# Kernel optimization log

Measured on AMD Instinct MI355X. Metric: run time of the kernel, lower is better.

## Reference

```python
import jax, jax.numpy as jnp
import numpy as np
import math

E = 1024      # embed_dim
H = 16        # num_heads
D = 32        # head_dim = E // H // 2
DEPTH = 12
LAMBDA_INIT = 0.8 - 0.6 * math.exp(-0.3 * DEPTH)
B, T = 4, 1024
EPS = 1e-5


def setup_inputs() -> dict:
    key = jax.random.key(0)
    ks = jax.random.split(key, 10)
    s = 0.02  # realistic init scale for weight matrices
    return {
        "x": jax.random.normal(ks[0], (B, T, E), jnp.float32),
        "Wq": jax.random.normal(ks[1], (E, E), jnp.float32) * s,
        "Wk": jax.random.normal(ks[2], (E, E), jnp.float32) * s,
        "Wv": jax.random.normal(ks[3], (E, E), jnp.float32) * s,
        "Wo": jax.random.normal(ks[4], (E, E), jnp.float32) * s,
        "lambda_q1": jax.random.normal(ks[5], (D,), jnp.float32) * 0.1,
        "lambda_k1": jax.random.normal(ks[6], (D,), jnp.float32) * 0.1,
        "lambda_q2": jax.random.normal(ks[7], (D,), jnp.float32) * 0.1,
        "lambda_k2": jax.random.normal(ks[8], (D,), jnp.float32) * 0.1,
        "g": jnp.ones((2 * D,), jnp.float32),  # subln affine weight
    }


def reference(x, Wq, Wk, Wv, Wo, lambda_q1, lambda_k1, lambda_q2, lambda_k2, g):
    b, t, _ = x.shape
    scaling = D ** -0.5
    # projections (torch Linear: x @ W.T), split into 2H half-width q/k heads
    q = (x @ Wq.T).reshape(b, t, 2 * H, D).transpose(0, 2, 1, 3) * scaling  # [b,2H,t,D]
    k = (x @ Wk.T).reshape(b, t, 2 * H, D).transpose(0, 2, 1, 3)            # [b,2H,t,D]
    v = (x @ Wv.T).reshape(b, t, H, 2 * D).transpose(0, 2, 1, 3)            # [b,H,t,2D]
    # dual score maps, fp32 softmax
    aw = jnp.einsum('bhqd,bhkd->bhqk', q, k)               # [b,2H,t,t]
    aw = jnp.nan_to_num(aw)
    aw = jax.nn.softmax(aw.astype(jnp.float32), axis=-1).astype(q.dtype)
    # scalar lambda
    lam1 = jnp.exp(jnp.sum(lambda_q1 * lambda_k1))
    lam2 = jnp.exp(jnp.sum(lambda_q2 * lambda_k2))
    lam = lam1 - lam2 + LAMBDA_INIT
    # differential subtract of the paired softmax maps
    aw = aw.reshape(b, H, 2, t, t)
    aw = aw[:, :, 0] - lam * aw[:, :, 1]                   # [b,H,t,t]
    attn = jnp.einsum('bhqk,bhkd->bhqd', aw, v)            # [b,H,t,2D]
    # per-head RMSNorm over 2D channel dim (affine)
    attn = attn * jax.lax.rsqrt(jnp.mean(attn * attn, axis=-1, keepdims=True) + EPS) * g
    attn = attn * (1.0 - LAMBDA_INIT)
    attn = attn.transpose(0, 2, 1, 3).reshape(b, t, H * 2 * D)  # [b,t,E]
    return attn @ Wo.T
```

## Files before the change

kernel.cpp:

```cpp
#include <hip/hip_runtime.h>
#include <math.h>

#define E_   1024
#define H_   16
#define B_   4
#define T_   1024
#define LAMBDA_INIT 0.783605766532f
#define SCALE_Q 0.17677669529663687f

typedef short s16x8 __attribute__((ext_vector_type(8)));
typedef float f32x4 __attribute__((ext_vector_type(4)));

__device__ inline ushort f2bf(float x) {
    unsigned u = __builtin_bit_cast(unsigned, x);
    u += 0x7fffu + ((u >> 16) & 1u);
    return (ushort)(u >> 16);
}

__device__ inline void gl_lds16(const ushort* g, ushort* l) {
    __builtin_amdgcn_global_load_lds((const __attribute__((address_space(1))) void*)g,
                                     (__attribute__((address_space(3))) void*)l,
                                     16, 0, 0);
}

__global__ __launch_bounds__(256) void cast_x(const float* __restrict__ in,
                                              ushort* __restrict__ out)
{
    int i = (blockIdx.x * 256 + threadIdx.x) * 8;
    float4 a = *(const float4*)&in[i];
    float4 b = *(const float4*)&in[i + 4];
    union { ushort u[8]; uint4 v; } o;
    o.u[0] = f2bf(a.x); o.u[1] = f2bf(a.y); o.u[2] = f2bf(a.z); o.u[3] = f2bf(a.w);
    o.u[4] = f2bf(b.x); o.u[5] = f2bf(b.y); o.u[6] = f2bf(b.z); o.u[7] = f2bf(b.w);
    *(uint4*)&out[i] = o.v;
}

__global__ __launch_bounds__(256) void cast_w4(
    const float* __restrict__ w0, const float* __restrict__ w1,
    const float* __restrict__ w2, const float* __restrict__ w3,
    ushort* __restrict__ o0, ushort* __restrict__ o1,
    ushort* __restrict__ o2, ushort* __restrict__ o3)
{
    const float* in = blockIdx.y == 0 ? w0 : (blockIdx.y == 1 ? w1 : (blockIdx.y == 2 ? w2 : w3));
    ushort* out = blockIdx.y == 0 ? o0 : (blockIdx.y == 1 ? o1 : (blockIdx.y == 2 ? o2 : o3));
    int i = (blockIdx.x * 256 + threadIdx.x) * 8;
    float4 a = *(const float4*)&in[i];
    float4 b = *(const float4*)&in[i + 4];
    union { ushort u[8]; uint4 v; } o;
    o.u[0] = f2bf(a.x); o.u[1] = f2bf(a.y); o.u[2] = f2bf(a.z); o.u[3] = f2bf(a.w);
    o.u[4] = f2bf(b.x); o.u[5] = f2bf(b.y); o.u[6] = f2bf(b.z); o.u[7] = f2bf(b.w);
    *(uint4*)&out[i] = o.v;
}

__global__ void lam_kernel(const float* __restrict__ lq1, const float* __restrict__ lk1,
                           const float* __restrict__ lq2, const float* __restrict__ lk2,
                           float* __restrict__ lamp)
{
    int l = threadIdx.x;
    float p1 = 0.f, p2 = 0.f;
    if (l < 32) { p1 = lq1[l] * lk1[l]; p2 = lq2[l] * lk2[l]; }
    #pragma unroll
    for (int off = 32; off; off >>= 1) {
        p1 += __shfl_xor(p1, off);
        p2 += __shfl_xor(p2, off);
    }
    if (l == 0) lamp[0] = expf(p1) - expf(p2) + LAMBDA_INIT;
}

__global__ __launch_bounds__(256) void gemm_qkv(
    const ushort* __restrict__ Xb, const ushort* __restrict__ Wqb,
    const ushort* __restrict__ Wkb, const ushort* __restrict__ Wvb,
    ushort* __restrict__ QKV)
{
    __shared__ ushort As[128 * 32];
    __shared__ ushort Ws[128 * 32];
    const int tid = threadIdx.x;
    const int wave = tid >> 6, lane = tid & 63;
    const int l15 = lane & 15, quad = lane >> 4;
    const int bm = blockIdx.y * 128;
    const int bng = blockIdx.x * 128;
    const int region = bng >> 10;
    const ushort* W = region == 0 ? Wqb : (region == 1 ? Wkb : Wvb);
    const float scale = region == 0 ? SCALE_Q : 1.0f;
    const int wn = bng & 1023;
    const int lrow = lane >> 2;
    const int lcol = (lane & 3) * 8;

    f32x4 acc[4][4] = {};
    const int wr = wave >> 1, wc = wave & 1;

    for (int k0 = 0; k0 < 1024; k0 += 32) {
        #pragma unroll
        for (int p = 0; p < 2; ++p) {
            int i = wave + 4 * p;
            gl_lds16(&Xb[(size_t)(bm + i * 16 + lrow) * 1024 + k0 + lcol], &As[i * 512]);
            gl_lds16(&W [(size_t)(wn + i * 16 + lrow) * 1024 + k0 + lcol], &Ws[i * 512]);
        }
        __syncthreads();
        s16x8 a[4], b[4];
        #pragma unroll
        for (int i = 0; i < 4; ++i)
            a[i] = *(const s16x8*)&As[(wr * 64 + i * 16 + l15) * 32 + quad * 8];
        #pragma unroll
        for (int j = 0; j < 4; ++j)
            b[j] = *(const s16x8*)&Ws[(wc * 64 + j * 16 + l15) * 32 + quad * 8];
        #pragma unroll
        for (int i = 0; i < 4; ++i)
            #pragma unroll
            for (int j = 0; j < 4; ++j)
                acc[i][j] = __builtin_amdgcn_mfma_f32_16x16x32_bf16(a[i], b[j], acc[i][j], 0, 0, 0);
        __syncthreads();
    }

    #pragma unroll
    for (int i = 0; i < 4; ++i)
        #pragma unroll
        for (int j = 0; j < 4; ++j)
            #pragma unroll
            for (int r = 0; r < 4; ++r) {
                int row = bm + wr * 64 + i * 16 + quad * 4 + r;
                int col = bng + wc * 64 + j * 16 + l15;
                QKV[(size_t)row * 3072 + col] = f2bf(acc[i][j][r] * scale);
            }
}

__global__ __launch_bounds__(256) void gemm_out(
    const ushort* __restrict__ Ab, const ushort* __restrict__ Wob,
    float* __restrict__ C)
{
    __shared__ ushort As[64 * 32];
    __shared__ ushort Ws[128 * 32];
    const int tid = threadIdx.x;
    const int wave = tid >> 6, lane = tid & 63;
    const int l15 = lane & 15, quad = lane >> 4;
    const int bm = blockIdx.y * 64;
    const int bn = blockIdx.x * 128;
    const int lrow = lane >> 2;
    const int lcol = (lane & 3) * 8;

    f32x4 acc[2][4] = {};
    const int wr = wave >> 1, wc = wave & 1;

    for (int k0 = 0; k0 < 1024; k0 += 32) {
        gl_lds16(&Ab[(size_t)(bm + wave * 16 + lrow) * 1024 + k0 + lcol], &As[wave * 512]);
        #pragma unroll
        for (int p = 0; p < 2; ++p) {
            int i = wave + 4 * p;
            gl_lds16(&Wob[(size_t)(bn + i * 16 + lrow) * 1024 + k0 + lcol], &Ws[i * 512]);
        }
        __syncthreads();
        s16x8 a[2], b[4];
        #pragma unroll
        for (int i = 0; i < 2; ++i)
            a[i] = *(const s16x8*)&As[(wr * 32 + i * 16 + l15) * 32 + quad * 8];
        #pragma unroll
        for (int j = 0; j < 4; ++j)
            b[j] = *(const s16x8*)&Ws[(wc * 64 + j * 16 + l15) * 32 + quad * 8];
        #pragma unroll
        for (int i = 0; i < 2; ++i)
            #pragma unroll
            for (int j = 0; j < 4; ++j)
                acc[i][j] = __builtin_amdgcn_mfma_f32_16x16x32_bf16(a[i], b[j], acc[i][j], 0, 0, 0);
        __syncthreads();
    }

    #pragma unroll
    for (int i = 0; i < 2; ++i)
        #pragma unroll
        for (int j = 0; j < 4; ++j)
            #pragma unroll
            for (int r = 0; r < 4; ++r) {
                int row = bm + wr * 32 + i * 16 + quad * 4 + r;
                int col = bn + wc * 64 + j * 16 + l15;
                C[(size_t)row * 1024 + col] = acc[i][j][r];
            }
}

__global__ __launch_bounds__(256) void diff_attn(
    const ushort* __restrict__ QKV, const float* __restrict__ g,
    const float* __restrict__ lamp, ushort* __restrict__ O)
{
    __shared__ __align__(16) ushort QsVt[64][72];
    __shared__ __align__(16) ushort Ks[64][72];
    __shared__ __align__(16) ushort Vs[64][72];
    __shared__ __align__(16) ushort Ps[4][16][72];

    const int tid  = threadIdx.x;
    const int lane = tid & 63;
    const int wave = tid >> 6;
    const int l15  = lane & 15;
    const int quad = lane >> 4;

    const int blk = blockIdx.x;
    const int qt = blk & 15;
    const int h  = (blk >> 4) & 15;
    const int b  = blk >> 8;
    const int q0 = qt * 64;
    const int hoff = h * 64;
    const size_t rowbase = (size_t)b * T_;

    const ushort* Qg = QKV;
    const ushort* Kg = QKV + 1024;
    const ushort* Vg = QKV + 2048;

    #pragma unroll
    for (int p = 0; p < 2; ++p) {
        int idx = tid + 256 * p;
        int r = idx >> 3, seg = idx & 7;
        *(uint4*)&QsVt[r][seg * 8] =
            *(const uint4*)&Qg[(rowbase + q0 + r) * 3072 + hoff + seg * 8];
    }
    const float lam = lamp[0];
    float gv[4];
    #pragma unroll
    for (int j = 0; j < 4; ++j) gv[j] = g[j * 16 + l15];
    __syncthreads();

    s16x8 aq[2];
    #pragma unroll
    for (int c = 0; c < 2; ++c)
        aq[c] = *(const s16x8*)&QsVt[wave * 16 + l15][c * 32 + quad * 8];

    const f32x4 zf = {0.f, 0.f, 0.f, 0.f};
    f32x4 o0[4] = {zf, zf, zf, zf};
    f32x4 o1[4] = {zf, zf, zf, zf};
    float lsum[2][4] = {};

    for (int kt = 0; kt < T_ / 64; ++kt) {
        __syncthreads();
        #pragma unroll
        for (int p = 0; p < 2; ++p) {
            int idx = tid + 256 * p;
            int r = idx >> 3, seg = idx & 7;
            size_t gro = (rowbase + kt * 64 + r) * 3072 + hoff + seg * 8;
            *(uint4*)&Ks[r][seg * 8] = *(const uint4*)&Kg[gro];
            *(uint4*)&Vs[r][seg * 8] = *(const uint4*)&Vg[gro];
        }
        __syncthreads();

        f32x4 S[2][4];
        #pragma unroll
        for (int c = 0; c < 2; ++c)
            #pragma unroll
            for (int j = 0; j < 4; ++j) {
                s16x8 bk = *(const s16x8*)&Ks[j * 16 + l15][c * 32 + quad * 8];
                S[c][j] = __builtin_amdgcn_mfma_f32_16x16x32_bf16(aq[c], bk, zf, 0, 0, 0);
            }

        #pragma unroll
        for (int p = 0; p < 2; ++p) {
            int idx = tid + 256 * p;
            int vc = idx & 63, n8 = (idx >> 6) * 8;
            union { ushort u[8]; uint4 v4; } tmp;
            #pragma unroll
            for (int i = 0; i < 8; ++i) tmp.u[i] = Vs[n8 + i][vc];
            *(uint4*)&QsVt[vc][n8] = tmp.v4;
        }
        __syncthreads();

        #pragma unroll
        for (int c = 0; c < 2; ++c) {
            #pragma unroll
            for (int j = 0; j < 4; ++j)
                #pragma unroll
                for (int r = 0; r < 4; ++r) {
                    float e = __expf(S[c][j][r]);
                    lsum[c][r] += e;
                    Ps[wave][quad * 4 + r][j * 16 + l15] = f2bf(e);
                }
            f32x4* oc = c ? o1 : o0;
            #pragma unroll
            for (int ch = 0; ch < 2; ++ch) {
                s16x8 pa = *(const s16x8*)&Ps[wave][l15][ch * 32 + quad * 8];
                #pragma unroll
                for (int j = 0; j < 4; ++j) {
                    s16x8 vbf = *(const s16x8*)&QsVt[j * 16 + l15][ch * 32 + quad * 8];
                    oc[j] = __builtin_amdgcn_mfma_f32_16x16x32_bf16(pa, vbf, oc[j], 0, 0, 0);
                }
            }
        }
    }

    #pragma unroll
    for (int c = 0; c < 2; ++c)
        #pragma unroll
        for (int r = 0; r < 4; ++r) {
            float s = lsum[c][r];
            s += __shfl_xor(s, 1); s += __shfl_xor(s, 2);
            s += __shfl_xor(s, 4); s += __shfl_xor(s, 8);
            lsum[c][r] = s;
        }

    float val[4][4];
    float ssq[4] = {0.f, 0.f, 0.f, 0.f};
    #pragma unroll
    for (int r = 0; r < 4; ++r) {
        float i0 = 1.f / lsum[0][r];
        float i1 = lam / lsum[1][r];
        #pragma unroll
        for (int j = 0; j < 4; ++j) {
            float v = o0[j][r] * i0 - o1[j][r] * i1;
            val[j][r] = v;
            ssq[r] += v * v;
        }
    }
    #pragma unroll
    for (int r = 0; r < 4; ++r) {
        float s = ssq[r];
        s += __shfl_xor(s, 1); s += __shfl_xor(s, 2);
        s += __shfl_xor(s, 4); s += __shfl_xor(s, 8);
        ssq[r] = rsqrtf(s * (1.f / 64.f) + 1e-5f);
    }
    const float fin = 1.f - LAMBDA_INIT;
    #pragma unroll
    for (int r = 0; r < 4; ++r)
        #pragma unroll
        for (int j = 0; j < 4; ++j)
            O[(rowbase + q0 + wave * 16 + quad * 4 + r) * 1024 + hoff + j * 16 + l15]
                = f2bf(val[j][r] * ssq[r] * gv[j] * fin);
}

extern "C" void kernel_launch(void* const* d_in, const int* in_sizes, int n_in,
                              void* d_out, int out_size, void* d_ws, size_t ws_size,
                              hipStream_t stream)
{
    const float* x   = (const float*)d_in[0];
    const float* Wq  = (const float*)d_in[1];
    const float* Wk  = (const float*)d_in[2];
    const float* Wv  = (const float*)d_in[3];
    const float* Wo  = (const float*)d_in[4];
    const float* lq1 = (const float*)d_in[5];
    const float* lk1 = (const float*)d_in[6];
    const float* lq2 = (const float*)d_in[7];
    const float* lk2 = (const float*)d_in[8];
    const float* g   = (const float*)d_in[9];
    float* out = (float*)d_out;

    const int M = B_ * T_;
    const size_t ME = (size_t)M * E_;
    const size_t EE = (size_t)E_ * E_;
    ushort* xb  = (ushort*)d_ws;
    ushort* Wqb = xb  + ME;
    ushort* Wkb = Wqb + EE;
    ushort* Wvb = Wkb + EE;
    ushort* Wob = Wvb + EE;
    ushort* QKV = Wob + EE;
    ushort* Ab  = QKV + (size_t)M * 3072;
    float*  lamp = (float*)(Ab + ME);

    cast_x<<<ME / (256 * 8), 256, 0, stream>>>(x, xb);
    cast_w4<<<dim3(EE / (256 * 8), 4), 256, 0, stream>>>(Wq, Wk, Wv, Wo, Wqb, Wkb, Wvb, Wob);
    lam_kernel<<<1, 64, 0, stream>>>(lq1, lk1, lq2, lk2, lamp);
    gemm_qkv<<<dim3(24, 32), 256, 0, stream>>>(xb, Wqb, Wkb, Wvb, QKV);
    diff_attn<<<B_ * H_ * (T_ / 64), 256, 0, stream>>>(QKV, g, lamp, Ab);
    gemm_out<<<dim3(8, 64), 256, 0, stream>>>(Ab, Wob, out);
}
```

Measured before the change: 216.3 us.

## Pre-transpose V in a separate kernel and drop per-tile LDS transpose in attention

Adds a transpose_v kernel that writes V in a [b, E, T] layout once, so the attention kernel loads V^T tiles directly instead of transposing V through shared memory for every key tile. This also removes one __syncthreads per iteration. K and V fragments are now hoisted into registers before the two score passes, and the Ps row padding changes from 72 to 68. The cost is an extra kernel launch, an extra workspace buffer, and an additional read and write of V, plus higher register pressure.

```diff
diff --git a/kernel.cpp b/kernel.cpp
--- a/kernel.cpp
+++ b/kernel.cpp
@@ -176,14 +176,43 @@
             }
 }
 
+__global__ __launch_bounds__(256) void transpose_v(
+    const ushort* __restrict__ QKV, ushort* __restrict__ Vt)
+{
+    __shared__ ushort Ls[64][72];
+    const int tid = threadIdx.x;
+    const int m0 = blockIdx.x * 64;
+    const int b  = m0 >> 10;
+    const int t0 = m0 & 1023;
+    const int e0 = blockIdx.y * 64;
+    #pragma unroll
+    for (int p = 0; p < 2; ++p) {
+        int idx = tid + 256 * p;
+        int r = idx >> 3, seg = (idx & 7) * 8;
+        *(uint4*)&Ls[r][seg] =
+            *(const uint4*)&QKV[(size_t)(m0 + r) * 3072 + 2048 + e0 + seg];
+    }
+    __syncthreads();
+    #pragma unroll
+    for (int p = 0; p < 2; ++p) {
+        int idx = tid + 256 * p;
+        int er = idx >> 3, ts = (idx & 7) * 8;
+        union { ushort u[8]; uint4 v; } o;
+        #pragma unroll
+        for (int i = 0; i < 8; ++i) o.u[i] = Ls[ts + i][er];
+        *(uint4*)&Vt[((size_t)b * E_ + e0 + er) * T_ + t0 + ts] = o.v;
+    }
+}
+
 __global__ __launch_bounds__(256) void diff_attn(
-    const ushort* __restrict__ QKV, const float* __restrict__ g,
-    const float* __restrict__ lamp, ushort* __restrict__ O)
-{
-    __shared__ __align__(16) ushort QsVt[64][72];
+    const ushort* __restrict__ QKV, const ushort* __restrict__ Vt,
+    const float* __restrict__ g, const float* __restrict__ lamp,
+    ushort* __restrict__ O)
+{
+    __shared__ __align__(16) ushort Qs[64][72];
     __shared__ __align__(16) ushort Ks[64][72];
-    __shared__ __align__(16) ushort Vs[64][72];
-    __shared__ __align__(16) ushort Ps[4][16][72];
+    __shared__ __align__(16) ushort Vts[64][72];
+    __shared__ __align__(16) ushort Ps[4][16][68];
 
     const int tid  = threadIdx.x;
     const int lane = tid & 63;
@@ -198,17 +227,17 @@
     const int q0 = qt * 64;
     const int hoff = h * 64;
     const size_t rowbase = (size_t)b * T_;
+    const size_t vtbase = ((size_t)b * E_ + hoff) * T_;
 
     const ushort* Qg = QKV;
     const ushort* Kg = QKV + 1024;
-    const ushort* Vg = QKV + 2048;
 
     #pragma unroll
     for (int p = 0; p < 2; ++p) {
         int idx = tid + 256 * p;
-        int r = idx >> 3, seg = idx & 7;
-        *(uint4*)&QsVt[r][seg * 8] =
-            *(const uint4*)&Qg[(rowbase + q0 + r) * 3072 + hoff + seg * 8];
+        int r = idx >> 3, seg = (idx & 7) * 8;
+        *(uint4*)&Qs[r][seg] =
+            *(const uint4*)&Qg[(rowbase + q0 + r) * 3072 + hoff + seg];
     }
     const float lam = lamp[0];
     float gv[4];
@@ -219,7 +248,7 @@
     s16x8 aq[2];
     #pragma unroll
     for (int c = 0; c < 2; ++c)
-        aq[c] = *(const s16x8*)&QsVt[wave * 16 + l15][c * 32 + quad * 8];
+        aq[c] = *(const s16x8*)&Qs[wave * 16 + l15][c * 32 + quad * 8];
 
     const f32x4 zf = {0.f, 0.f, 0.f, 0.f};
     f32x4 o0[4] = {zf, zf, zf, zf};
@@ -231,52 +260,45 @@
         #pragma unroll
         for (int p = 0; p < 2; ++p) {
             int idx = tid + 256 * p;
-            int r = idx >> 3, seg = idx & 7;
-            size_t gro = (rowbase + kt * 64 + r) * 3072 + hoff + seg * 8;
-            *(uint4*)&Ks[r][seg * 8] = *(const uint4*)&Kg[gro];
-            *(uint4*)&Vs[r][seg * 8] = *(const uint4*)&Vg[gro];
-        }
-        __syncthreads();
-
-        f32x4 S[2][4];
-        #pragma unroll
-        for (int c = 0; c < 2; ++c)
-            #pragma unroll
-            for (int j = 0; j < 4; ++j) {
-                s16x8 bk = *(const s16x8*)&Ks[j * 16 + l15][c * 32 + quad * 8];
-                S[c][j] = __builtin_amdgcn_mfma_f32_16x16x32_bf16(aq[c], bk, zf, 0, 0, 0);
-            }
-
-        #pragma unroll
-        for (int p = 0; p < 2; ++p) {
-            int idx = tid + 256 * p;
-            int vc = idx & 63, n8 = (idx >> 6) * 8;
-            union { ushort u[8]; uint4 v4; } tmp;
-            #pragma unroll
-            for (int i = 0; i < 8; ++i) tmp.u[i] = Vs[n8 + i][vc];
-            *(uint4*)&QsVt[vc][n8] = tmp.v4;
-        }
-        __syncthreads();
+            int r = idx >> 3, seg = (idx & 7) * 8;
+            *(uint4*)&Ks[r][seg] =
+                *(const uint4*)&Kg[(rowbase + kt * 64 + r) * 3072 + hoff + seg];
+            *(uint4*)&Vts[r][seg] =
+                *(const uint4*)&Vt[vtbase + (size_t)r * T_ + kt * 64 + seg];
+        }
+        __syncthreads();
+
+        s16x8 bk0[4], bk1[4], vt0[4], vt1[4];
+        #pragma unroll
+        for (int j = 0; j < 4; ++j) {
+            bk0[j] = *(const s16x8*)&Ks [j * 16 + l15][     quad * 8];
+            bk1[j] = *(const s16x8*)&Ks [j * 16 + l15][32 + quad * 8];
+            vt0[j] = *(const s16x8*)&Vts[j * 16 + l15][     quad * 8];
+            vt1[j] = *(const s16x8*)&Vts[j * 16 + l15][32 + quad * 8];
+        }
 
         #pragma unroll
         for (int c = 0; c < 2; ++c) {
+            f32x4 S[4];
+            #pragma unroll
+            for (int j = 0; j < 4; ++j)
+                S[j] = __builtin_amdgcn_mfma_f32_16x16x32_bf16(
+                    aq[c], c ? bk1[j] : bk0[j], zf, 0, 0, 0);
             #pragma unroll
             for (int j = 0; j < 4; ++j)
                 #pragma unroll
                 for (int r = 0; r < 4; ++r) {
-                    float e = __expf(S[c][j][r]);
+                    float e = __expf(S[j][r]);
                     lsum[c][r] += e;
                     Ps[wave][quad * 4 + r][j * 16 + l15] = f2bf(e);
                 }
+            s16x8 pa0 = *(const s16x8*)&Ps[wave][l15][     quad * 8];
+            s16x8 pa1 = *(const s16x8*)&Ps[wave][l15][32 + quad * 8];
             f32x4* oc = c ? o1 : o0;
             #pragma unroll
-            for (int ch = 0; ch < 2; ++ch) {
-                s16x8 pa = *(const s16x8*)&Ps[wave][l15][ch * 32 + quad * 8];
-                #pragma unroll
-                for (int j = 0; j < 4; ++j) {
-                    s16x8 vbf = *(const s16x8*)&QsVt[j * 16 + l15][ch * 32 + quad * 8];
-                    oc[j] = __builtin_amdgcn_mfma_f32_16x16x32_bf16(pa, vbf, oc[j], 0, 0, 0);
-                }
+            for (int j = 0; j < 4; ++j) {
+                oc[j] = __builtin_amdgcn_mfma_f32_16x16x32_bf16(pa0, vt0[j], oc[j], 0, 0, 0);
+                oc[j] = __builtin_amdgcn_mfma_f32_16x16x32_bf16(pa1, vt1[j], oc[j], 0, 0, 0);
             }
         }
     }
@@ -345,13 +367,15 @@
     ushort* Wvb = Wkb + EE;
     ushort* Wob = Wvb + EE;
     ushort* QKV = Wob + EE;
-    ushort* Ab  = QKV + (size_t)M * 3072;
+    ushort* Vtb = QKV + (size_t)M * 3072;
+    ushort* Ab  = Vtb + ME;
     float*  lamp = (float*)(Ab + ME);
 
     cast_x<<<ME / (256 * 8), 256, 0, stream>>>(x, xb);
     cast_w4<<<dim3(EE / (256 * 8), 4), 256, 0, stream>>>(Wq, Wk, Wv, Wo, Wqb, Wkb, Wvb, Wob);
     lam_kernel<<<1, 64, 0, stream>>>(lq1, lk1, lq2, lk2, lamp);
     gemm_qkv<<<dim3(24, 32), 256, 0, stream>>>(xb, Wqb, Wkb, Wvb, QKV);
-    diff_attn<<<B_ * H_ * (T_ / 64), 256, 0, stream>>>(QKV, g, lamp, Ab);
+    transpose_v<<<dim3(M / 64, E_ / 64), 256, 0, stream>>>(QKV, Vtb);
+    diff_attn<<<B_ * H_ * (T_ / 64), 256, 0, stream>>>(QKV, Vtb, g, lamp, Ab);
     gemm_out<<<dim3(8, 64), 256, 0, stream>>>(Ab, Wob, out);
 }
```

Measured after the change: 220.5 us. About the same (+1.9%).
